# Kernel optimization log

Hardware: AMD Instinct MI355X
Metric: run time of the kernel (lower is better)

The kernel has to match this reference:

```python
import jax, jax.numpy as jnp
import numpy as np

N = 100000
METADATA = [128, 64, 32, 16]   # channels per degree l = 0..3
N_INV = METADATA[0]            # 128 invariant (l=0) channels
NUM_CH = sum(METADATA)         # 240 total channels
DIM = sum(m * (2 * l + 1) for l, m in enumerate(METADATA))  # 592 columns
EPS = 1e-5


def make_rep_layout():
    # column -> channel index, channels ordered by degree
    segs, off = [], 0
    for l, m in enumerate(METADATA):
        segs.append(np.repeat(np.arange(m) + off, 2 * l + 1))
        off += m
    return jnp.asarray(np.concatenate(segs), dtype=jnp.int64)


def setup_inputs() -> dict:
    key = jax.random.key(0)
    ks = jax.random.split(key, 5)
    ten = jax.random.normal(ks[0], (N, DIM), dtype=jnp.float32)
    w1 = jax.random.normal(ks[1], (NUM_CH, N_INV), dtype=jnp.float32) / np.sqrt(NUM_CH)
    w2 = jax.random.normal(ks[2], (N_INV, N_INV), dtype=jnp.float32) / np.sqrt(N_INV)
    w3 = jax.random.normal(ks[3], (N_INV, N_INV), dtype=jnp.float32) / np.sqrt(N_INV)
    return {
        "ten": ten,
        "rep_layout": make_rep_layout(),
        "w1": w1,
        "g1": jnp.ones((N_INV,), jnp.float32),
        "beta1": jnp.zeros((N_INV,), jnp.float32),
        "w2": w2,
        "b2": jnp.zeros((N_INV,), jnp.float32),
        "g2": jnp.ones((N_INV,), jnp.float32),
        "beta2": jnp.zeros((N_INV,), jnp.float32),
        "w3": w3,
        "b3": jnp.zeros((N_INV,), jnp.float32),
    }


def _layernorm(x, g, b):
    mu = jnp.mean(x, axis=-1, keepdims=True)
    var = jnp.var(x, axis=-1, keepdims=True)
    return (x - mu) * jax.lax.rsqrt(var + EPS) * g + b


def reference(ten, rep_layout, w1, g1, beta1, w2, b2, g2, beta2, w3, b3):
    # --- EvNorm1d (n_invariant_channels > 0 branch) ---
    x10 = ten[:, :N_INV]                         # [N, 128] invariant part
    eq = ten[:, N_INV:]                          # [N, 464] equivariant part
    seg = rep_layout[N_INV:] - N_INV             # column -> eq channel (0..111)
    n_eq = NUM_CH - N_INV                        # 112 equivariant channels
    # segment sum of squares over columns, keyed by channel
    sumsq = jax.ops.segment_sum((eq * eq).T, seg, num_segments=n_eq).T  # [N, 112]
    divisor = jnp.sqrt(sumsq + 1.0)
    x11 = divisor - 1.0
    x1 = jnp.concatenate([x10, x11], axis=1)     # [N, 240]
    x2 = eq / divisor[:, seg]                    # broadcast-divide via gather
    # --- MLP on invariant content ---
    h = x1 @ w1                                  # Linear(240->128, no bias)
    h = _layernorm(h, g1, beta1)
    h = h @ w2 + b2
    h = jax.nn.silu(h)
    h = _layernorm(h, g2, beta2)
    h = h @ w3 + b3
    return jnp.concatenate([h, x2], axis=-1)     # [N, 592]
```

## Files before the change

kernel.cpp:

```cpp
#include <hip/hip_runtime.h>

#define NROWS   100000
#define DIM     592
#define NINV    128
#define NEQ     112
#define NCH     240
#define ROWS    64
#define BLK     256
#define HOFF    8192
#define GRID    ((NROWS + ROWS - 1) / ROWS)

typedef float f32x4 __attribute__((ext_vector_type(4)));

__device__ __forceinline__ int swz(int q, int r) {
    return (q & ~3) | ((q ^ (r >> 3)) & 3);
}

__global__ __launch_bounds__(BLK, 2)
void evmlp_kernel(const float* __restrict__ ten,
                  const float* __restrict__ w1,
                  const float* __restrict__ g1,
                  const float* __restrict__ be1,
                  const float* __restrict__ w2,
                  const float* __restrict__ b2,
                  const float* __restrict__ g2,
                  const float* __restrict__ be2,
                  const float* __restrict__ w3,
                  const float* __restrict__ b3,
                  float* __restrict__ out)
{
    __shared__ __align__(16) float lds[16384];

    const int t  = threadIdx.x;
    const int r0 = blockIdx.x * ROWS;

    #pragma unroll
    for (int it = 0; it < 8; ++it) {
        int i = t + it * BLK;
        int r = i >> 5, q = i & 31;
        int rd = r0 + r; if (rd >= NROWS) rd = NROWS - 1;
        f32x4 v = *(const f32x4*)(ten + (size_t)rd * DIM + (q << 2));
        *(f32x4*)(lds + r * NCH + (swz(q, r) << 2)) = v;
    }

    for (int i = t; i < ROWS * NEQ; i += BLK) {
        int r = i / NEQ, c = i - r * NEQ;
        int rd = r0 + r; const bool valid = rd < NROWS; if (!valid) rd = NROWS - 1;
        int base, nc;
        if (c < 64)      { base = 3 * c;              nc = 3; }
        else if (c < 96) { base = 192 + 5 * (c - 64); nc = 5; }
        else             { base = 352 + 7 * (c - 96); nc = 7; }
        const float* p = ten + (size_t)rd * DIM + NINV + base;
        float vals[7]; float ssq = 1.0f;
        for (int j = 0; j < nc; ++j) { float v = p[j]; vals[j] = v; ssq += v * v; }
        float dv = sqrtf(ssq), inv = 1.0f / dv;
        int k = NINV + c;
        lds[r * NCH + (swz(k >> 2, r) << 2) + (k & 3)] = dv - 1.0f;
        if (valid) {
            float* po = out + (size_t)rd * DIM + NINV + base;
            for (int j = 0; j < nc; ++j) po[j] = vals[j] * inv;
        }
    }
    __syncthreads();

    const int cgrp = t & 15;
    const int rgrp = (t >> 4) & 7;
    const int kg   = t >> 7;
    const int rr   = rgrp << 3;
    const int par  = rgrp & 1;
    const int qA   = 2 * cgrp + par;
    const int qB   = 2 * cgrp + 1 - par;
    const int colA = qA << 2;
    const int colB = qB << 2;

    float acc[8][8];

    auto zero_acc = [&]() {
        #pragma unroll
        for (int i = 0; i < 8; ++i)
            #pragma unroll
            for (int j = 0; j < 8; ++j) acc[i][j] = 0.f;
    };

    auto run_gemm = [&](const float* __restrict__ w, const float* xb, int xstride,
                        int kbase, int kn) {
        #pragma unroll 2
        for (int kc = 0; kc < kn; kc += 4) {
            const int k0 = kbase + kc;
            const int pg = swz(k0 >> 2, rr) << 2;
            f32x4 xv[8];
            #pragma unroll
            for (int i = 0; i < 8; ++i)
                xv[i] = *(const f32x4*)(xb + (rr + i) * xstride + pg);
            #pragma unroll
            for (int kk = 0; kk < 4; ++kk) {
                f32x4 wa = *(const f32x4*)(w + (size_t)(k0 + kk) * NINV + colA);
                f32x4 wb = *(const f32x4*)(w + (size_t)(k0 + kk) * NINV + colB);
                #pragma unroll
                for (int i = 0; i < 8; ++i) {
                    const float x = xv[i][kk];
                    acc[i][0] += x * wa[0]; acc[i][1] += x * wa[1];
                    acc[i][2] += x * wa[2]; acc[i][3] += x * wa[3];
                    acc[i][4] += x * wb[0]; acc[i][5] += x * wb[1];
                    acc[i][6] += x * wb[2]; acc[i][7] += x * wb[3];
                }
            }
        }
    };

    auto put_partial = [&]() {
        const int io = 4 * (1 - kg);
        #pragma unroll
        for (int i2 = 0; i2 < 4; ++i2) {
            const int r = rr + io + i2;
            f32x4 a = { acc[io+i2][0], acc[io+i2][1], acc[io+i2][2], acc[io+i2][3] };
            f32x4 b = { acc[io+i2][4], acc[io+i2][5], acc[io+i2][6], acc[io+i2][7] };
            *(f32x4*)(lds + r * NINV + (swz(qA, r) << 2)) = a;
            *(f32x4*)(lds + r * NINV + (swz(qB, r) << 2)) = b;
        }
    };

    zero_acc();
    run_gemm(w1, lds, NCH, kg * 120, 120);
    __syncthreads();
    put_partial();
    __syncthreads();
    {
        const int io = 4 * kg;
        f32x4 ga = *(const f32x4*)(g1 + colA), gb = *(const f32x4*)(g1 + colB);
        f32x4 ba = *(const f32x4*)(be1 + colA), bb = *(const f32x4*)(be1 + colB);
        #pragma unroll
        for (int i2 = 0; i2 < 4; ++i2) {
            const int r = rr + io + i2;
            f32x4 pa = *(const f32x4*)(lds + r * NINV + (swz(qA, r) << 2));
            f32x4 pb = *(const f32x4*)(lds + r * NINV + (swz(qB, r) << 2));
            float v[8];
            #pragma unroll
            for (int j = 0; j < 4; ++j) {
                v[j]     = acc[io+i2][j]     + pa[j];
                v[4 + j] = acc[io+i2][4 + j] + pb[j];
            }
            float s = 0.f, s2 = 0.f;
            #pragma unroll
            for (int j = 0; j < 8; ++j) { s += v[j]; s2 += v[j] * v[j]; }
            #pragma unroll
            for (int off = 1; off < 16; off <<= 1) {
                s  += __shfl_xor(s,  off);
                s2 += __shfl_xor(s2, off);
            }
            const float mu   = s * (1.f / 128.f);
            const float rstd = rsqrtf(s2 * (1.f / 128.f) - mu * mu + 1e-5f);
            f32x4 ha, hb;
            #pragma unroll
            for (int j = 0; j < 4; ++j) {
                ha[j] = (v[j]     - mu) * rstd * ga[j] + ba[j];
                hb[j] = (v[4 + j] - mu) * rstd * gb[j] + bb[j];
            }
            *(f32x4*)(lds + HOFF + r * NINV + (swz(qA, r) << 2)) = ha;
            *(f32x4*)(lds + HOFF + r * NINV + (swz(qB, r) << 2)) = hb;
        }
    }
    __syncthreads();

    zero_acc();
    run_gemm(w2, lds + HOFF, NINV, kg * 64, 64);
    put_partial();
    __syncthreads();
    {
        const int io = 4 * kg;
        f32x4 ga  = *(const f32x4*)(g2 + colA),  gb  = *(const f32x4*)(g2 + colB);
        f32x4 ba  = *(const f32x4*)(be2 + colA), bb  = *(const f32x4*)(be2 + colB);
        f32x4 b2a = *(const f32x4*)(b2 + colA),  b2b = *(const f32x4*)(b2 + colB);
        #pragma unroll
        for (int i2 = 0; i2 < 4; ++i2) {
            const int r = rr + io + i2;
            f32x4 pa = *(const f32x4*)(lds + r * NINV + (swz(qA, r) << 2));
            f32x4 pb = *(const f32x4*)(lds + r * NINV + (swz(qB, r) << 2));
            float v[8];
            #pragma unroll
            for (int j = 0; j < 4; ++j) {
                float x0 = acc[io+i2][j]     + pa[j] + b2a[j];
                float x1 = acc[io+i2][4 + j] + pb[j] + b2b[j];
                v[j]     = x0 / (1.f + __expf(-x0));
                v[4 + j] = x1 / (1.f + __expf(-x1));
            }
            float s = 0.f, s2 = 0.f;
            #pragma unroll
            for (int j = 0; j < 8; ++j) { s += v[j]; s2 += v[j] * v[j]; }
            #pragma unroll
            for (int off = 1; off < 16; off <<= 1) {
                s  += __shfl_xor(s,  off);
                s2 += __shfl_xor(s2, off);
            }
            const float mu   = s * (1.f / 128.f);
            const float rstd = rsqrtf(s2 * (1.f / 128.f) - mu * mu + 1e-5f);
            f32x4 ha, hb;
            #pragma unroll
            for (int j = 0; j < 4; ++j) {
                ha[j] = (v[j]     - mu) * rstd * ga[j] + ba[j];
                hb[j] = (v[4 + j] - mu) * rstd * gb[j] + bb[j];
            }
            *(f32x4*)(lds + HOFF + r * NINV + (swz(qA, r) << 2)) = ha;
            *(f32x4*)(lds + HOFF + r * NINV + (swz(qB, r) << 2)) = hb;
        }
    }
    __syncthreads();

    zero_acc();
    run_gemm(w3, lds + HOFF, NINV, kg * 64, 64);
    put_partial();
    __syncthreads();
    {
        const int io = 4 * kg;
        f32x4 b3a = *(const f32x4*)(b3 + colA), b3b = *(const f32x4*)(b3 + colB);
        #pragma unroll
        for (int i2 = 0; i2 < 4; ++i2) {
            const int r  = rr + io + i2;
            const int rd = r0 + r;
            f32x4 pa = *(const f32x4*)(lds + r * NINV + (swz(qA, r) << 2));
            f32x4 pb = *(const f32x4*)(lds + r * NINV + (swz(qB, r) << 2));
            f32x4 oa, ob;
            #pragma unroll
            for (int j = 0; j < 4; ++j) {
                oa[j] = acc[io+i2][j]     + pa[j] + b3a[j];
                ob[j] = acc[io+i2][4 + j] + pb[j] + b3b[j];
            }
            if (rd < NROWS) {
                *(f32x4*)(out + (size_t)rd * DIM + colA) = oa;
                *(f32x4*)(out + (size_t)rd * DIM + colB) = ob;
            }
        }
    }
}

extern "C" void kernel_launch(void* const* d_in, const int* in_sizes, int n_in,
                              void* d_out, int out_size, void* d_ws, size_t ws_size,
                              hipStream_t stream) {
    const float* ten = (const float*)d_in[0];
    const float* w1  = (const float*)d_in[2];
    const float* g1  = (const float*)d_in[3];
    const float* be1 = (const float*)d_in[4];
    const float* w2  = (const float*)d_in[5];
    const float* b2  = (const float*)d_in[6];
    const float* g2  = (const float*)d_in[7];
    const float* be2 = (const float*)d_in[8];
    const float* w3  = (const float*)d_in[9];
    const float* b3  = (const float*)d_in[10];
    float* out = (float*)d_out;

    dim3 grid(GRID);
    dim3 block(BLK);
    evmlp_kernel<<<grid, block, 0, stream>>>(ten, w1, g1, be1, w2, b2, g2, be2, w3, b3, out);
}
```

Measured before the change: 828.6 us.

## Halve row tile to 32 and shrink per-thread tile for higher occupancy

```diff
diff --git a/kernel.cpp b/kernel.cpp
--- a/kernel.cpp
+++ b/kernel.cpp
@@ -5,10 +5,11 @@
 #define NINV    128
 #define NEQ     112
 #define NCH     240
-#define ROWS    64
+#define ROWS    32
 #define BLK     256
-#define HOFF    8192
-#define GRID    ((NROWS + ROWS - 1) / ROWS)
+#define LDSF    8192
+#define POFF    4096
+#define GRID    (NROWS / ROWS)
 
 typedef float f32x4 __attribute__((ext_vector_type(4)));
 
@@ -16,7 +17,7 @@
     return (q & ~3) | ((q ^ (r >> 3)) & 3);
 }
 
-__global__ __launch_bounds__(BLK, 2)
+__global__ __launch_bounds__(BLK, 4)
 void evmlp_kernel(const float* __restrict__ ten,
                   const float* __restrict__ w1,
                   const float* __restrict__ g1,
@@ -29,62 +30,53 @@
                   const float* __restrict__ b3,
                   float* __restrict__ out)
 {
-    __shared__ __align__(16) float lds[16384];
+    __shared__ __align__(16) float lds[LDSF];
 
     const int t  = threadIdx.x;
     const int r0 = blockIdx.x * ROWS;
 
     #pragma unroll
-    for (int it = 0; it < 8; ++it) {
+    for (int it = 0; it < 4; ++it) {
         int i = t + it * BLK;
         int r = i >> 5, q = i & 31;
-        int rd = r0 + r; if (rd >= NROWS) rd = NROWS - 1;
-        f32x4 v = *(const f32x4*)(ten + (size_t)rd * DIM + (q << 2));
+        f32x4 v = *(const f32x4*)(ten + (size_t)(r0 + r) * DIM + (q << 2));
         *(f32x4*)(lds + r * NCH + (swz(q, r) << 2)) = v;
     }
 
     for (int i = t; i < ROWS * NEQ; i += BLK) {
         int r = i / NEQ, c = i - r * NEQ;
-        int rd = r0 + r; const bool valid = rd < NROWS; if (!valid) rd = NROWS - 1;
         int base, nc;
         if (c < 64)      { base = 3 * c;              nc = 3; }
         else if (c < 96) { base = 192 + 5 * (c - 64); nc = 5; }
         else             { base = 352 + 7 * (c - 96); nc = 7; }
-        const float* p = ten + (size_t)rd * DIM + NINV + base;
+        const float* p = ten + (size_t)(r0 + r) * DIM + NINV + base;
         float vals[7]; float ssq = 1.0f;
         for (int j = 0; j < nc; ++j) { float v = p[j]; vals[j] = v; ssq += v * v; }
         float dv = sqrtf(ssq), inv = 1.0f / dv;
         int k = NINV + c;
         lds[r * NCH + (swz(k >> 2, r) << 2) + (k & 3)] = dv - 1.0f;
-        if (valid) {
-            float* po = out + (size_t)rd * DIM + NINV + base;
-            for (int j = 0; j < nc; ++j) po[j] = vals[j] * inv;
-        }
-    }
-    __syncthreads();
-
-    const int cgrp = t & 15;
-    const int rgrp = (t >> 4) & 7;
+        float* po = out + (size_t)(r0 + r) * DIM + NINV + base;
+        for (int j = 0; j < nc; ++j) po[j] = vals[j] * inv;
+    }
+    __syncthreads();
+
+    const int cgrp = t & 31;
+    const int rgrp = (t >> 5) & 3;
     const int kg   = t >> 7;
     const int rr   = rgrp << 3;
-    const int par  = rgrp & 1;
-    const int qA   = 2 * cgrp + par;
-    const int qB   = 2 * cgrp + 1 - par;
-    const int colA = qA << 2;
-    const int colB = qB << 2;
-
-    float acc[8][8];
+    const int c0   = cgrp << 2;
+
+    float acc[8][4];
 
     auto zero_acc = [&]() {
         #pragma unroll
         for (int i = 0; i < 8; ++i)
             #pragma unroll
-            for (int j = 0; j < 8; ++j) acc[i][j] = 0.f;
+            for (int j = 0; j < 4; ++j) acc[i][j] = 0.f;
     };
 
     auto run_gemm = [&](const float* __restrict__ w, const float* xb, int xstride,
                         int kbase, int kn) {
-        #pragma unroll 2
         for (int kc = 0; kc < kn; kc += 4) {
             const int k0 = kbase + kc;
             const int pg = swz(k0 >> 2, rr) << 2;
@@ -92,19 +84,20 @@
             #pragma unroll
             for (int i = 0; i < 8; ++i)
                 xv[i] = *(const f32x4*)(xb + (rr + i) * xstride + pg);
-            #pragma unroll
-            for (int kk = 0; kk < 4; ++kk) {
-                f32x4 wa = *(const f32x4*)(w + (size_t)(k0 + kk) * NINV + colA);
-                f32x4 wb = *(const f32x4*)(w + (size_t)(k0 + kk) * NINV + colB);
+            f32x4 wv[4];
+            #pragma unroll
+            for (int kk = 0; kk < 4; ++kk)
+                wv[kk] = *(const f32x4*)(w + (size_t)(k0 + kk) * NINV + c0);
+            #pragma unroll
+            for (int kk = 0; kk < 4; ++kk)
                 #pragma unroll
                 for (int i = 0; i < 8; ++i) {
                     const float x = xv[i][kk];
-                    acc[i][0] += x * wa[0]; acc[i][1] += x * wa[1];
-                    acc[i][2] += x * wa[2]; acc[i][3] += x * wa[3];
-                    acc[i][4] += x * wb[0]; acc[i][5] += x * wb[1];
-                    acc[i][6] += x * wb[2]; acc[i][7] += x * wb[3];
+                    acc[i][0] += x * wv[kk][0];
+                    acc[i][1] += x * wv[kk][1];
+                    acc[i][2] += x * wv[kk][2];
+                    acc[i][3] += x * wv[kk][3];
                 }
-            }
         }
     };
 
@@ -113,10 +106,9 @@
         #pragma unroll
         for (int i2 = 0; i2 < 4; ++i2) {
             const int r = rr + io + i2;
-            f32x4 a = { acc[io+i2][0], acc[io+i2][1], acc[io+i2][2], acc[io+i2][3] };
-            f32x4 b = { acc[io+i2][4], acc[io+i2][5], acc[io+i2][6], acc[io+i2][7] };
-            *(f32x4*)(lds + r * NINV + (swz(qA, r) << 2)) = a;
-            *(f32x4*)(lds + r * NINV + (swz(qB, r) << 2)) = b;
+            f32x4 a = { acc[io + i2][0], acc[io + i2][1],
+                        acc[io + i2][2], acc[io + i2][3] };
+            *(f32x4*)(lds + POFF + r * NINV + (swz(cgrp, r) << 2)) = a;
         }
     };
 
@@ -127,108 +119,85 @@
     __syncthreads();
     {
         const int io = 4 * kg;
-        f32x4 ga = *(const f32x4*)(g1 + colA), gb = *(const f32x4*)(g1 + colB);
-        f32x4 ba = *(const f32x4*)(be1 + colA), bb = *(const f32x4*)(be1 + colB);
-        #pragma unroll
-        for (int i2 = 0; i2 < 4; ++i2) {
-            const int r = rr + io + i2;
-            f32x4 pa = *(const f32x4*)(lds + r * NINV + (swz(qA, r) << 2));
-            f32x4 pb = *(const f32x4*)(lds + r * NINV + (swz(qB, r) << 2));
-            float v[8];
-            #pragma unroll
-            for (int j = 0; j < 4; ++j) {
-                v[j]     = acc[io+i2][j]     + pa[j];
-                v[4 + j] = acc[io+i2][4 + j] + pb[j];
-            }
+        f32x4 gv = *(const f32x4*)(g1 + c0);
+        f32x4 bv = *(const f32x4*)(be1 + c0);
+        #pragma unroll
+        for (int i2 = 0; i2 < 4; ++i2) {
+            const int r = rr + io + i2;
+            f32x4 pv = *(const f32x4*)(lds + POFF + r * NINV + (swz(cgrp, r) << 2));
+            float v[4];
+            #pragma unroll
+            for (int j = 0; j < 4; ++j) v[j] = acc[io + i2][j] + pv[j];
             float s = 0.f, s2 = 0.f;
             #pragma unroll
-            for (int j = 0; j < 8; ++j) { s += v[j]; s2 += v[j] * v[j]; }
-            #pragma unroll
-            for (int off = 1; off < 16; off <<= 1) {
+            for (int j = 0; j < 4; ++j) { s += v[j]; s2 += v[j] * v[j]; }
+            #pragma unroll
+            for (int off = 1; off < 32; off <<= 1) {
                 s  += __shfl_xor(s,  off);
                 s2 += __shfl_xor(s2, off);
             }
             const float mu   = s * (1.f / 128.f);
             const float rstd = rsqrtf(s2 * (1.f / 128.f) - mu * mu + 1e-5f);
-            f32x4 ha, hb;
-            #pragma unroll
-            for (int j = 0; j < 4; ++j) {
-                ha[j] = (v[j]     - mu) * rstd * ga[j] + ba[j];
-                hb[j] = (v[4 + j] - mu) * rstd * gb[j] + bb[j];
-            }
-            *(f32x4*)(lds + HOFF + r * NINV + (swz(qA, r) << 2)) = ha;
-            *(f32x4*)(lds + HOFF + r * NINV + (swz(qB, r) << 2)) = hb;
+            f32x4 h;
+            #pragma unroll
+            for (int j = 0; j < 4; ++j) h[j] = (v[j] - mu) * rstd * gv[j] + bv[j];
+            *(f32x4*)(lds + r * NINV + (swz(cgrp, r) << 2)) = h;
         }
     }
     __syncthreads();
 
     zero_acc();
-    run_gemm(w2, lds + HOFF, NINV, kg * 64, 64);
+    run_gemm(w2, lds, NINV, kg * 64, 64);
     put_partial();
     __syncthreads();
     {
         const int io = 4 * kg;
-        f32x4 ga  = *(const f32x4*)(g2 + colA),  gb  = *(const f32x4*)(g2 + colB);
-        f32x4 ba  = *(const f32x4*)(be2 + colA), bb  = *(const f32x4*)(be2 + colB);
-        f32x4 b2a = *(const f32x4*)(b2 + colA),  b2b = *(const f32x4*)(b2 + colB);
-        #pragma unroll
-        for (int i2 = 0; i2 < 4; ++i2) {
-            const int r = rr + io + i2;
-            f32x4 pa = *(const f32x4*)(lds + r * NINV + (swz(qA, r) << 2));
-            f32x4 pb = *(const f32x4*)(lds + r * NINV + (swz(qB, r) << 2));
-            float v[8];
+        f32x4 gv  = *(const f32x4*)(g2 + c0);
+        f32x4 bv  = *(const f32x4*)(be2 + c0);
+        f32x4 b2v = *(const f32x4*)(b2 + c0);
+        #pragma unroll
+        for (int i2 = 0; i2 < 4; ++i2) {
+            const int r = rr + io + i2;
+            f32x4 pv = *(const f32x4*)(lds + POFF + r * NINV + (swz(cgrp, r) << 2));
+            float v[4];
             #pragma unroll
             for (int j = 0; j < 4; ++j) {
-                float x0 = acc[io+i2][j]     + pa[j] + b2a[j];
-                float x1 = acc[io+i2][4 + j] + pb[j] + b2b[j];
-                v[j]     = x0 / (1.f + __expf(-x0));
-                v[4 + j] = x1 / (1.f + __expf(-x1));
+                float x0 = acc[io + i2][j] + pv[j] + b2v[j];
+                v[j] = x0 / (1.f + __expf(-x0));
             }
             float s = 0.f, s2 = 0.f;
             #pragma unroll
-            for (int j = 0; j < 8; ++j) { s += v[j]; s2 += v[j] * v[j]; }
-            #pragma unroll
-            for (int off = 1; off < 16; off <<= 1) {
+            for (int j = 0; j < 4; ++j) { s += v[j]; s2 += v[j] * v[j]; }
+            #pragma unroll
+            for (int off = 1; off < 32; off <<= 1) {
                 s  += __shfl_xor(s,  off);
                 s2 += __shfl_xor(s2, off);
             }
             const float mu   = s * (1.f / 128.f);
             const float rstd = rsqrtf(s2 * (1.f / 128.f) - mu * mu + 1e-5f);
-            f32x4 ha, hb;
-            #pragma unroll
-            for (int j = 0; j < 4; ++j) {
-                ha[j] = (v[j]     - mu) * rstd * ga[j] + ba[j];
-                hb[j] = (v[4 + j] - mu) * rstd * gb[j] + bb[j];
-            }
-            *(f32x4*)(lds + HOFF + r * NINV + (swz(qA, r) << 2)) = ha;
-            *(f32x4*)(lds + HOFF + r * NINV + (swz(qB, r) << 2)) = hb;
+            f32x4 h;
+            #pragma unroll
+            for (int j = 0; j < 4; ++j) h[j] = (v[j] - mu) * rstd * gv[j] + bv[j];
+            *(f32x4*)(lds + r * NINV + (swz(cgrp, r) << 2)) = h;
         }
     }
     __syncthreads();
 
     zero_acc();
-    run_gemm(w3, lds + HOFF, NINV, kg * 64, 64);
+    run_gemm(w3, lds, NINV, kg * 64, 64);
     put_partial();
     __syncthreads();
     {
         const int io = 4 * kg;
-        f32x4 b3a = *(const f32x4*)(b3 + colA), b3b = *(const f32x4*)(b3 + colB);
-        #pragma unroll
-        for (int i2 = 0; i2 < 4; ++i2) {
-            const int r  = rr + io + i2;
-            const int rd = r0 + r;
-            f32x4 pa = *(const f32x4*)(lds + r * NINV + (swz(qA, r) << 2));
-            f32x4 pb = *(const f32x4*)(lds + r * NINV + (swz(qB, r) << 2));
-            f32x4 oa, ob;
-            #pragma unroll
-            for (int j = 0; j < 4; ++j) {
-                oa[j] = acc[io+i2][j]     + pa[j] + b3a[j];
-                ob[j] = acc[io+i2][4 + j] + pb[j] + b3b[j];
-            }
-            if (rd < NROWS) {
-                *(f32x4*)(out + (size_t)rd * DIM + colA) = oa;
-                *(f32x4*)(out + (size_t)rd * DIM + colB) = ob;
-            }
+        f32x4 b3v = *(const f32x4*)(b3 + c0);
+        #pragma unroll
+        for (int i2 = 0; i2 < 4; ++i2) {
+            const int r = rr + io + i2;
+            f32x4 pv = *(const f32x4*)(lds + POFF + r * NINV + (swz(cgrp, r) << 2));
+            f32x4 o;
+            #pragma unroll
+            for (int j = 0; j < 4; ++j) o[j] = acc[io + i2][j] + pv[j] + b3v[j];
+            *(f32x4*)(out + (size_t)(r0 + r) * DIM + c0) = o;
         }
     }
 }
```

Result: no change. 815.7 us (-1.6%).
